# Performance work log

Hardware: AMD Instinct MI355X
Metric: run time of the kernel (lower is better)

The kernel has to match this reference:

```python
import jax, jax.numpy as jnp
import numpy as np

# SMPL-X kinematic tree (55 joints): 22 body, jaw, 2 eyes, 15 left-hand, 15 right-hand
PARENTS = np.array([-1, 0, 0, 0, 1, 2, 3, 4, 5, 6, 7, 8, 9, 9, 9, 12, 13, 14, 16, 17, 18, 19,
                    15, 15, 15,
                    20, 25, 26, 20, 28, 29, 20, 31, 32, 20, 34, 35, 20, 37, 38,
                    21, 40, 41, 21, 43, 44, 21, 46, 47, 21, 49, 50, 21, 52, 53])
V = 10475   # SMPL-X vertex count
J = 55      # joints
NB = 10     # betas
PF = 54 * 9 # pose-feature dim
B, L = 4, 128


def axis_angle_to_matrix(aa):
    # aa: (..., 3) -> (..., 3, 3) via Rodrigues' formula
    angle = jnp.sqrt(jnp.sum(aa * aa, axis=-1, keepdims=True) + 1e-12)  # (...,1)
    axis = aa / angle
    x, y, z = axis[..., 0], axis[..., 1], axis[..., 2]
    zero = jnp.zeros_like(x)
    K = jnp.stack([jnp.stack([zero, -z, y], -1),
                   jnp.stack([z, zero, -x], -1),
                   jnp.stack([-y, x, zero], -1)], axis=-2)           # (...,3,3)
    s = jnp.sin(angle)[..., None]
    c = jnp.cos(angle)[..., None]
    eye = jnp.eye(3, dtype=aa.dtype)
    outer = axis[..., :, None] * axis[..., None, :]
    return c * eye + s * K + (1.0 - c) * outer


def batch_rigid_transform(rot_mats, joints):
    # rot_mats: (..., J, 3, 3), joints: (..., J, 3) -> rel_transforms (..., J, 4, 4)
    rel = jnp.concatenate([joints[..., :1, :],
                           joints[..., 1:, :] - joints[..., PARENTS[1:], :]], axis=-2)
    top = jnp.concatenate([rot_mats, rel[..., None]], axis=-1)        # (...,J,3,4)
    bottom = jnp.broadcast_to(jnp.array([0., 0., 0., 1.], top.dtype),
                              top.shape[:-2] + (1, 4))
    tmats = jnp.concatenate([top, bottom], axis=-2)                   # (...,J,4,4)
    chain = [tmats[..., 0, :, :]]
    for i in range(1, J):  # fixed 55-joint tree dependency
        chain.append(chain[PARENTS[i]] @ tmats[..., i, :, :])
    T = jnp.stack(chain, axis=-3)                                     # (...,J,4,4)
    corr = jnp.einsum('...jcd,...jd->...jc', T[..., :3, :3], joints)
    return T.at[..., :3, 3].add(-corr)


def setup_inputs() -> dict:
    key = jax.random.key(0)
    ks = jax.random.split(key, 11)
    w = jax.random.uniform(ks[8], (V, J), dtype=jnp.float32)
    lbs_weights = w / jnp.sum(w, axis=-1, keepdims=True)
    return {
        'body_pose': 0.3 * jax.random.normal(ks[0], (B, L, 63), jnp.float32),
        'betas': jax.random.normal(ks[1], (B, L, NB), jnp.float32),
        'global_orient': 0.3 * jax.random.normal(ks[2], (B, L, 3), jnp.float32),
        'transl': jax.random.normal(ks[3], (B, L, 3), jnp.float32),
        'v_template': 0.5 * jax.random.normal(ks[4], (V, 3), jnp.float32),
        'shapedirs': 0.01 * jax.random.normal(ks[5], (V, 3, NB), jnp.float32),
        'posedirs': 0.01 * jax.random.normal(ks[6], (PF, V, 3), jnp.float32),
        'lbs_weights': lbs_weights,
        'J_template': 0.3 * jax.random.normal(ks[7], (J, 3), jnp.float32),
        'J_shapedirs': 0.01 * jax.random.normal(ks[9], (J, 3, NB), jnp.float32),
        'other_default_pose': 0.1 * jax.random.normal(ks[10], (99,), jnp.float32),
    }


def reference(body_pose, betas, global_orient, transl, v_template, shapedirs,
              posedirs, lbs_weights, J_template, J_shapedirs, other_default_pose):
    prefix = body_pose.shape[:-1]
    odp = jnp.broadcast_to(other_default_pose, prefix + (99,))
    full_pose = jnp.concatenate([global_orient, body_pose, odp], axis=-1)  # (B,L,165)
    rot_mats = axis_angle_to_matrix(full_pose.reshape(prefix + (J, 3)))    # (B,L,55,3,3)
    # fast skeleton
    joints = J_template + jnp.einsum('...k,jck->...jc', betas, J_shapedirs)  # (B,L,55,3)
    A = batch_rigid_transform(rot_mats, joints)                              # (B,L,55,4,4)
    eye = jnp.eye(3, dtype=rot_mats.dtype)
    pose_feature = (rot_mats[..., 1:, :, :] - eye).reshape(prefix + (PF,))
    v_posed = (v_template
               + jnp.einsum('...k,vck->...vc', betas, shapedirs)
               + jnp.einsum('...k,kvc->...vc', pose_feature, posedirs))      # (B,L,V,3)
    T = jnp.einsum('vj,...jcd->...vcd', lbs_weights, A)                      # (B,L,V,4,4)
    verts = (jnp.einsum('...vcd,...vd->...vc', T[..., :3, :3], v_posed)
             + T[..., :3, 3])
    return verts + transl[..., None, :]
```

## Files before the change

kernel.cpp:

```cpp
#include <hip/hip_runtime.h>

#define V_CNT   10475
#define N3      31425
#define NPAD    31488
#define J_CNT   55
#define NBETA   10
#define KP      512
#define NFRAMES 512
#define BM      64
#define BNC     192
#define VTILES  164
#define FTILES  8

typedef __attribute__((ext_vector_type(8))) __bf16 bf16x8;
typedef __attribute__((ext_vector_type(8))) unsigned short ushort8;
typedef __attribute__((ext_vector_type(4))) float f32x4;

__device__ __forceinline__ unsigned short f2bf(float f) {
    unsigned u = __float_as_uint(f);
    u += 0x7fff + ((u >> 16) & 1);
    return (unsigned short)(u >> 16);
}
__device__ __forceinline__ float bf2f(unsigned short s) {
    return __uint_as_float(((unsigned)s) << 16);
}
__device__ __forceinline__ void gl_lds16(const void* g, void* l) {
    auto gp = (const __attribute__((address_space(1))) unsigned int*)(uintptr_t)g;
    auto lp = (__attribute__((address_space(3))) unsigned int*)(unsigned int)(uintptr_t)l;
    __builtin_amdgcn_global_load_lds(gp, lp, 16, 0, 0);
}

__device__ __constant__ int c_parents[J_CNT] = {
    -1, 0, 0, 0, 1, 2, 3, 4, 5, 6, 7, 8, 9, 9, 9, 12, 13, 14, 16, 17, 18, 19,
    15, 15, 15,
    20, 25, 26, 20, 28, 29, 20, 31, 32, 20, 34, 35, 20, 37, 38,
    21, 40, 41, 21, 43, 44, 21, 46, 47, 21, 49, 50, 21, 52, 53};

__global__ __launch_bounds__(64) void skel_kernel(
    const float* __restrict__ body_pose, const float* __restrict__ betas,
    const float* __restrict__ global_orient, const float* __restrict__ J_template,
    const float* __restrict__ J_shapedirs, const float* __restrict__ odp,
    unsigned short* __restrict__ pf_ext, unsigned short* __restrict__ A_bf)
{
    const int n = blockIdx.x;
    const int lane = threadIdx.x;
    __shared__ float R_s[J_CNT][9];
    __shared__ float j_s[J_CNT][3];
    __shared__ float G_s[J_CNT][12];

    if (lane < J_CNT) {
        float aa0, aa1, aa2;
        if (lane == 0) {
            aa0 = global_orient[n * 3 + 0];
            aa1 = global_orient[n * 3 + 1];
            aa2 = global_orient[n * 3 + 2];
        } else if (lane < 22) {
            int o = n * 63 + (lane - 1) * 3;
            aa0 = body_pose[o]; aa1 = body_pose[o + 1]; aa2 = body_pose[o + 2];
        } else {
            int o = (lane - 22) * 3;
            aa0 = odp[o]; aa1 = odp[o + 1]; aa2 = odp[o + 2];
        }
        float ang = sqrtf(aa0 * aa0 + aa1 * aa1 + aa2 * aa2 + 1e-12f);
        float inv = 1.0f / ang;
        float ax = aa0 * inv, ay = aa1 * inv, az = aa2 * inv;
        float s = sinf(ang), c = cosf(ang), cc = 1.0f - c;
        float R[9];
        R[0] = c + cc * ax * ax;        R[1] = -s * az + cc * ax * ay;  R[2] = s * ay + cc * ax * az;
        R[3] = s * az + cc * ax * ay;   R[4] = c + cc * ay * ay;        R[5] = -s * ax + cc * ay * az;
        R[6] = -s * ay + cc * ax * az;  R[7] = s * ax + cc * ay * az;   R[8] = c + cc * az * az;
#pragma unroll
        for (int k = 0; k < 9; k++) R_s[lane][k] = R[k];
#pragma unroll
        for (int cd = 0; cd < 3; cd++) {
            float acc = J_template[lane * 3 + cd];
#pragma unroll
            for (int k = 0; k < NBETA; k++)
                acc += betas[n * NBETA + k] * J_shapedirs[(lane * 3 + cd) * NBETA + k];
            j_s[lane][cd] = acc;
        }
        if (lane >= 1) {
#pragma unroll
            for (int e = 0; e < 9; e++)
                pf_ext[n * KP + (lane - 1) * 9 + e] =
                    f2bf(R[e] - ((e == 0 || e == 4 || e == 8) ? 1.0f : 0.0f));
        }
    }
    if (lane == 55) {
#pragma unroll
        for (int b = 0; b < NBETA; b++) pf_ext[n * KP + 486 + b] = f2bf(betas[n * NBETA + b]);
        pf_ext[n * KP + 496] = 0x3F80;
    }
    if (lane == 56) {
        for (int k = 497; k < KP; k++) pf_ext[n * KP + k] = 0;
    }
    __syncthreads();
    if (lane == 0) {
        for (int r = 0; r < 3; r++) {
            G_s[0][r * 4 + 0] = R_s[0][r * 3 + 0];
            G_s[0][r * 4 + 1] = R_s[0][r * 3 + 1];
            G_s[0][r * 4 + 2] = R_s[0][r * 3 + 2];
            G_s[0][r * 4 + 3] = j_s[0][r];
        }
        for (int i = 1; i < J_CNT; i++) {
            int p = c_parents[i];
            float rel0 = j_s[i][0] - j_s[p][0];
            float rel1 = j_s[i][1] - j_s[p][1];
            float rel2 = j_s[i][2] - j_s[p][2];
            for (int r = 0; r < 3; r++) {
                float g0 = G_s[p][r * 4 + 0], g1 = G_s[p][r * 4 + 1], g2 = G_s[p][r * 4 + 2];
                G_s[i][r * 4 + 0] = g0 * R_s[i][0] + g1 * R_s[i][3] + g2 * R_s[i][6];
                G_s[i][r * 4 + 1] = g0 * R_s[i][1] + g1 * R_s[i][4] + g2 * R_s[i][7];
                G_s[i][r * 4 + 2] = g0 * R_s[i][2] + g1 * R_s[i][5] + g2 * R_s[i][8];
                G_s[i][r * 4 + 3] = g0 * rel0 + g1 * rel1 + g2 * rel2 + G_s[p][r * 4 + 3];
            }
        }
    }
    __syncthreads();
    float vals[12];
#pragma unroll
    for (int r = 0; r < 12; r++) vals[r] = 0.0f;
    if (lane < J_CNT) {
        const float jx = j_s[lane][0], jy = j_s[lane][1], jz = j_s[lane][2];
#pragma unroll
        for (int r = 0; r < 3; r++) {
            float g0 = G_s[lane][r * 4 + 0], g1 = G_s[lane][r * 4 + 1], g2 = G_s[lane][r * 4 + 2];
            vals[r * 4 + 0] = g0;
            vals[r * 4 + 1] = g1;
            vals[r * 4 + 2] = g2;
            vals[r * 4 + 3] = G_s[lane][r * 4 + 3] - (g0 * jx + g1 * jy + g2 * jz);
        }
    }
#pragma unroll
    for (int r = 0; r < 12; r++)
        A_bf[(n * 12 + r) * 64 + lane] = f2bf(vals[r]);
}

__global__ __launch_bounds__(256) void repack_kernel(
    const float* __restrict__ posedirs, const float* __restrict__ shapedirs,
    const float* __restrict__ v_template, unsigned short* __restrict__ B_pack)
{
    __shared__ float t[64][65];
    const int n0 = blockIdx.x * 64, k0 = blockIdx.y * 64;
    const int tn = threadIdx.x & 63, tk4 = threadIdx.x >> 6;
#pragma unroll
    for (int rep = 0; rep < 16; rep++) {
        int kl = rep * 4 + tk4;
        int kg = k0 + kl, ng = n0 + tn;
        float v = 0.0f;
        if (ng < N3) {
            if (kg < 486)       v = posedirs[(size_t)kg * N3 + ng];
            else if (kg < 496)  v = shapedirs[ng * NBETA + (kg - 486)];
            else if (kg == 496) v = v_template[ng];
        }
        t[kl][tn] = v;
    }
    __syncthreads();
#pragma unroll
    for (int rep = 0; rep < 2; rep++) {
        int nl = rep * 32 + (threadIdx.x >> 3);
        int kg = threadIdx.x & 7;
        ushort8 val;
#pragma unroll
        for (int j = 0; j < 8; j++) val[j] = f2bf(t[kg * 8 + j][nl]);
        *(ushort8*)(&B_pack[(size_t)(n0 + nl) * KP + k0 + kg * 8]) = val;
    }
}

__global__ __launch_bounds__(256, 2) void gemm_kernel(
    const unsigned short* __restrict__ pf_ext, const unsigned short* __restrict__ B_pack,
    const unsigned short* __restrict__ A_bf, const float* __restrict__ lbs_weights,
    const float* __restrict__ transl, float* __restrict__ out)
{
    __shared__ __align__(128) unsigned char smem[74496];
    unsigned char* pf_b0 = smem;
    unsigned char* pf_b1 = smem + 8192;
    unsigned char* B_b0  = smem + 16384;
    unsigned char* B_b1  = smem + 40960;
    unsigned char* w_b   = smem + 65536;
    float* tr_s          = (float*)(smem + 73728);
    unsigned short* vp_s = (unsigned short*)(smem + 16384);
    float* rst           = (float*)(smem + 41472);

    const int tid = threadIdx.x;
    const int w = tid >> 6, l = tid & 63;
    const int wm = w >> 1, wn = w & 1;

    const int bid = blockIdx.x;
    const int group = bid >> 6, gi = bid & 63;
    int vt, ft;
    if (group < 20) { vt = group * 8 + (gi & 7); ft = gi >> 3; }
    else            { vt = 160 + (gi & 3);       ft = gi >> 2; }
    const int f0 = ft * BM;
    const int v00 = vt * 64;
    const int n0c = vt * BNC;

    {
        int v = tid >> 2, jg = tid & 3;
        int vg = v00 + v;
#pragma unroll
        for (int h = 0; h < 2; h++) {
            ushort8 val;
#pragma unroll
            for (int e = 0; e < 8; e++) {
                int j = jg * 16 + h * 8 + e;
                float f = (vg < V_CNT && j < J_CNT) ? lbs_weights[vg * J_CNT + j] : 0.0f;
                val[e] = f2bf(f);
            }
            int chunk = (jg * 2 + h) ^ (v & 7);
            *(ushort8*)(w_b + v * 128 + chunk * 16) = val;
        }
    }
    if (tid < 192) tr_s[tid] = transl[f0 * 3 + tid];

    const unsigned char* pfg = (const unsigned char*)pf_ext + (size_t)f0 * (KP * 2);
    const unsigned char* Bg  = (const unsigned char*)B_pack + (size_t)n0c * (KP * 2);

#define STAGE_KS(ks, pfd, Bd)                                                              \
    {                                                                                      \
        const int kb = (ks) * 128;                                                         \
        _Pragma("unroll")                                                                  \
        for (int i = 0; i < 2; i++) {                                                      \
            int row0 = w * 16 + i * 8;                                                     \
            int row = row0 + (l >> 3);                                                     \
            const unsigned char* src = pfg + (size_t)row * (KP * 2) + kb +                 \
                                       (((l & 7) ^ (l >> 3)) * 16);                        \
            gl_lds16(src, (pfd) + row0 * 128);                                             \
        }                                                                                  \
        _Pragma("unroll")                                                                  \
        for (int i = 0; i < 6; i++) {                                                      \
            int row0 = i * 32 + w * 8;                                                     \
            int row = row0 + (l >> 3);                                                     \
            const unsigned char* src = Bg + (size_t)row * (KP * 2) + kb +                  \
                                       (((l & 7) ^ (l >> 3)) * 16);                        \
            gl_lds16(src, (Bd) + row0 * 128);                                              \
        }                                                                                  \
    }

    f32x4 acc[2][6];
#pragma unroll
    for (int m = 0; m < 2; m++)
#pragma unroll
        for (int nn = 0; nn < 6; nn++) acc[m][nn] = (f32x4){0.f, 0.f, 0.f, 0.f};

    STAGE_KS(0, pf_b0, B_b0);
    STAGE_KS(1, pf_b1, B_b1);
    asm volatile("s_waitcnt vmcnt(8)" ::: "memory");
    __builtin_amdgcn_sched_barrier(0);
    __builtin_amdgcn_s_barrier();

#pragma unroll
    for (int ks = 0; ks < 8; ks++) {
        unsigned char* pfc = (ks & 1) ? pf_b1 : pf_b0;
        unsigned char* Bc  = (ks & 1) ? B_b1 : B_b0;
#pragma unroll
        for (int ksub = 0; ksub < 2; ksub++) {
            bf16x8 a[2], b[6];
#pragma unroll
            for (int m = 0; m < 2; m++) {
                int f = wm * 32 + m * 16 + (l & 15);
                int off = f * 128 + ((ksub * 64 + (l >> 4) * 16) ^ ((f & 7) << 4));
                a[m] = *(const bf16x8*)(pfc + off);
            }
#pragma unroll
            for (int nn = 0; nn < 6; nn++) {
                int col = wn * 96 + nn * 16 + (l & 15);
                int off = col * 128 + ((ksub * 64 + (l >> 4) * 16) ^ ((col & 7) << 4));
                b[nn] = *(const bf16x8*)(Bc + off);
            }
#pragma unroll
            for (int m = 0; m < 2; m++)
#pragma unroll
                for (int nn = 0; nn < 6; nn++)
                    acc[m][nn] = __builtin_amdgcn_mfma_f32_16x16x32_bf16(a[m], b[nn], acc[m][nn], 0, 0, 0);
        }
        __builtin_amdgcn_sched_barrier(0);
        __builtin_amdgcn_s_barrier();
        if (ks < 6) {
            STAGE_KS(ks + 2, pfc, Bc);
        }
        if (ks < 7) {
            if (ks < 6) asm volatile("s_waitcnt vmcnt(8)" ::: "memory");
            else        asm volatile("s_waitcnt vmcnt(0)" ::: "memory");
            __builtin_amdgcn_sched_barrier(0);
            __builtin_amdgcn_s_barrier();
        }
    }
#undef STAGE_KS

#pragma unroll
    for (int m = 0; m < 2; m++)
#pragma unroll
        for (int nn = 0; nn < 6; nn++)
#pragma unroll
            for (int e = 0; e < 4; e++) {
                int f = wm * 32 + m * 16 + (l >> 4) * 4 + e;
                int col = wn * 96 + nn * 16 + (l & 15);
                vp_s[f * 196 + col] = f2bf(acc[m][nn][e]);
            }
    __syncthreads();

    const unsigned char* Ab = (const unsigned char*)A_bf;
    float res[3][8][2];
#pragma unroll
    for (int c = 0; c < 3; c++) {
        f32x4 acc2[8][2];
#pragma unroll
        for (int m = 0; m < 8; m++)
#pragma unroll
            for (int nn = 0; nn < 2; nn++) acc2[m][nn] = (f32x4){0.f, 0.f, 0.f, 0.f};
#pragma unroll
        for (int ksub = 0; ksub < 2; ksub++) {
            bf16x8 bw[2];
#pragma unroll
            for (int nn = 0; nn < 2; nn++) {
                int v = wn * 32 + nn * 16 + (l & 15);
                int off = v * 128 + ((ksub * 64 + (l >> 4) * 16) ^ ((v & 7) << 4));
                bw[nn] = *(const bf16x8*)(w_b + off);
            }
#pragma unroll
            for (int m = 0; m < 8; m++) {
                int row16 = l & 15;
                int f_rel = m * 4 + (row16 >> 2);
                int rr = row16 & 3;
                const unsigned char* asrc = Ab +
                    ((size_t)((f0 + wm * 32 + f_rel) * 12 + c * 4 + rr)) * 128 +
                    ksub * 64 + (l >> 4) * 16;
                bf16x8 af = *(const bf16x8*)asrc;
                acc2[m][0] = __builtin_amdgcn_mfma_f32_16x16x32_bf16(af, bw[0], acc2[m][0], 0, 0, 0);
                acc2[m][1] = __builtin_amdgcn_mfma_f32_16x16x32_bf16(af, bw[1], acc2[m][1], 0, 0, 0);
            }
        }
#pragma unroll
        for (int m = 0; m < 8; m++)
#pragma unroll
            for (int nn = 0; nn < 2; nn++) {
                int f_rel = wm * 32 + m * 4 + (l >> 4);
                int vloc = wn * 32 + nn * 16 + (l & 15);
                float d0 = bf2f(vp_s[f_rel * 196 + vloc * 3 + 0]);
                float d1 = bf2f(vp_s[f_rel * 196 + vloc * 3 + 1]);
                float d2 = bf2f(vp_s[f_rel * 196 + vloc * 3 + 2]);
                f32x4 tt = acc2[m][nn];
                res[c][m][nn] = tt[0] * d0 + tt[1] * d1 + tt[2] * d2 + tt[3] + tr_s[f_rel * 3 + c];
            }
    }

    const int olim = N3 - v00 * 3;
#pragma unroll
    for (int chunk = 0; chunk < 2; chunk++) {
        __syncthreads();
        if (wm == chunk) {
#pragma unroll
            for (int m = 0; m < 8; m++)
#pragma unroll
                for (int nn = 0; nn < 2; nn++) {
                    int r = m * 4 + (l >> 4);
                    int colv = (wn * 32 + nn * 16 + (l & 15)) * 3;
#pragma unroll
                    for (int c = 0; c < 3; c++)
                        rst[r * 200 + colv + c] = res[c][m][nn];
                }
        }
        __syncthreads();
        size_t base = ((size_t)(f0 + chunk * 32) * V_CNT + v00) * 3;
#pragma unroll
        for (int k = 0; k < 24; k++) {
            int i = tid + k * 256;
            int r = i / 192;
            int o = i - r * 192;
            if (o < olim)
                out[base + (size_t)r * N3 + o] = rst[r * 200 + o];
        }
    }
}

extern "C" void kernel_launch(void* const* d_in, const int* in_sizes, int n_in,
                              void* d_out, int out_size, void* d_ws, size_t ws_size,
                              hipStream_t stream)
{
    const float* body_pose     = (const float*)d_in[0];
    const float* betas         = (const float*)d_in[1];
    const float* global_orient = (const float*)d_in[2];
    const float* transl        = (const float*)d_in[3];
    const float* v_template    = (const float*)d_in[4];
    const float* shapedirs     = (const float*)d_in[5];
    const float* posedirs      = (const float*)d_in[6];
    const float* lbs_weights   = (const float*)d_in[7];
    const float* J_template    = (const float*)d_in[8];
    const float* J_shapedirs   = (const float*)d_in[9];
    const float* odp           = (const float*)d_in[10];
    float* out = (float*)d_out;

    unsigned short* B_pack = (unsigned short*)d_ws;
    unsigned short* pf_ext = (unsigned short*)((char*)d_ws + 32243712);
    unsigned short* A_bf   = (unsigned short*)((char*)d_ws + 32243712 + 524288);

    dim3 rgrid(NPAD / 64, KP / 64);
    repack_kernel<<<rgrid, 256, 0, stream>>>(posedirs, shapedirs, v_template, B_pack);

    skel_kernel<<<NFRAMES, 64, 0, stream>>>(body_pose, betas, global_orient,
                                            J_template, J_shapedirs, odp,
                                            pf_ext, A_bf);

    gemm_kernel<<<VTILES * FTILES, 256, 0, stream>>>(pf_ext, B_pack, A_bf, lbs_weights,
                                                     transl, out);
}
```

Measured before the change: 116.5 us.

## Load pose-feature operand directly into registers and shrink shared memory footprint

```diff
diff --git a/kernel.cpp b/kernel.cpp
--- a/kernel.cpp
+++ b/kernel.cpp
@@ -172,15 +172,13 @@
     const unsigned short* __restrict__ A_bf, const float* __restrict__ lbs_weights,
     const float* __restrict__ transl, float* __restrict__ out)
 {
-    __shared__ __align__(128) unsigned char smem[74496];
-    unsigned char* pf_b0 = smem;
-    unsigned char* pf_b1 = smem + 8192;
-    unsigned char* B_b0  = smem + 16384;
-    unsigned char* B_b1  = smem + 40960;
-    unsigned char* w_b   = smem + 65536;
-    float* tr_s          = (float*)(smem + 73728);
-    unsigned short* vp_s = (unsigned short*)(smem + 16384);
-    float* rst           = (float*)(smem + 41472);
+    __shared__ __align__(128) unsigned char smem[49920];
+    unsigned char* B_b0  = smem;
+    unsigned char* B_b1  = smem + 24576;
+    float* tr_s          = (float*)(smem + 49152);
+    unsigned short* vp_s = (unsigned short*)(smem);
+    unsigned char* w_b   = smem + 25600;
+    float* rst           = (float*)(smem);
 
     const int tid = threadIdx.x;
     const int w = tid >> 6, l = tid & 63;
@@ -195,38 +193,14 @@
     const int v00 = vt * 64;
     const int n0c = vt * BNC;
 
-    {
-        int v = tid >> 2, jg = tid & 3;
-        int vg = v00 + v;
-#pragma unroll
-        for (int h = 0; h < 2; h++) {
-            ushort8 val;
-#pragma unroll
-            for (int e = 0; e < 8; e++) {
-                int j = jg * 16 + h * 8 + e;
-                float f = (vg < V_CNT && j < J_CNT) ? lbs_weights[vg * J_CNT + j] : 0.0f;
-                val[e] = f2bf(f);
-            }
-            int chunk = (jg * 2 + h) ^ (v & 7);
-            *(ushort8*)(w_b + v * 128 + chunk * 16) = val;
-        }
-    }
     if (tid < 192) tr_s[tid] = transl[f0 * 3 + tid];
 
     const unsigned char* pfg = (const unsigned char*)pf_ext + (size_t)f0 * (KP * 2);
     const unsigned char* Bg  = (const unsigned char*)B_pack + (size_t)n0c * (KP * 2);
 
-#define STAGE_KS(ks, pfd, Bd)                                                              \
+#define STAGE_B(ks, Bd)                                                                    \
     {                                                                                      \
         const int kb = (ks) * 128;                                                         \
-        _Pragma("unroll")                                                                  \
-        for (int i = 0; i < 2; i++) {                                                      \
-            int row0 = w * 16 + i * 8;                                                     \
-            int row = row0 + (l >> 3);                                                     \
-            const unsigned char* src = pfg + (size_t)row * (KP * 2) + kb +                 \
-                                       (((l & 7) ^ (l >> 3)) * 16);                        \
-            gl_lds16(src, (pfd) + row0 * 128);                                             \
-        }                                                                                  \
         _Pragma("unroll")                                                                  \
         for (int i = 0; i < 6; i++) {                                                      \
             int row0 = i * 32 + w * 8;                                                     \
@@ -236,6 +210,17 @@
             gl_lds16(src, (Bd) + row0 * 128);                                              \
         }                                                                                  \
     }
+#define PF_LOAD(ks, dst)                                                                   \
+    {                                                                                      \
+        _Pragma("unroll")                                                                  \
+        for (int m = 0; m < 2; m++)                                                        \
+            _Pragma("unroll")                                                              \
+            for (int ksub = 0; ksub < 2; ksub++) {                                         \
+                int row = wm * 32 + m * 16 + (l & 15);                                     \
+                (dst)[m][ksub] = *(const bf16x8*)(pfg + (size_t)row * 1024 +               \
+                                                  (ks) * 128 + ksub * 64 + (l >> 4) * 16); \
+            }                                                                              \
+    }
 
     f32x4 acc[2][6];
 #pragma unroll
@@ -243,25 +228,22 @@
 #pragma unroll
         for (int nn = 0; nn < 6; nn++) acc[m][nn] = (f32x4){0.f, 0.f, 0.f, 0.f};
 
-    STAGE_KS(0, pf_b0, B_b0);
-    STAGE_KS(1, pf_b1, B_b1);
-    asm volatile("s_waitcnt vmcnt(8)" ::: "memory");
+    bf16x8 pfR[2][2][2];
+
+    PF_LOAD(0, pfR[0]);
+    PF_LOAD(1, pfR[1]);
+    STAGE_B(0, B_b0);
+    STAGE_B(1, B_b1);
+    asm volatile("s_waitcnt vmcnt(6)" ::: "memory");
     __builtin_amdgcn_sched_barrier(0);
     __builtin_amdgcn_s_barrier();
 
 #pragma unroll
     for (int ks = 0; ks < 8; ks++) {
-        unsigned char* pfc = (ks & 1) ? pf_b1 : pf_b0;
-        unsigned char* Bc  = (ks & 1) ? B_b1 : B_b0;
+        unsigned char* Bc = (ks & 1) ? B_b1 : B_b0;
 #pragma unroll
         for (int ksub = 0; ksub < 2; ksub++) {
-            bf16x8 a[2], b[6];
-#pragma unroll
-            for (int m = 0; m < 2; m++) {
-                int f = wm * 32 + m * 16 + (l & 15);
-                int off = f * 128 + ((ksub * 64 + (l >> 4) * 16) ^ ((f & 7) << 4));
-                a[m] = *(const bf16x8*)(pfc + off);
-            }
+            bf16x8 b[6];
 #pragma unroll
             for (int nn = 0; nn < 6; nn++) {
                 int col = wn * 96 + nn * 16 + (l & 15);
@@ -272,22 +254,41 @@
             for (int m = 0; m < 2; m++)
 #pragma unroll
                 for (int nn = 0; nn < 6; nn++)
-                    acc[m][nn] = __builtin_amdgcn_mfma_f32_16x16x32_bf16(a[m], b[nn], acc[m][nn], 0, 0, 0);
+                    acc[m][nn] = __builtin_amdgcn_mfma_f32_16x16x32_bf16(
+                        pfR[ks & 1][m][ksub], b[nn], acc[m][nn], 0, 0, 0);
         }
         __builtin_amdgcn_sched_barrier(0);
         __builtin_amdgcn_s_barrier();
         if (ks < 6) {
-            STAGE_KS(ks + 2, pfc, Bc);
+            PF_LOAD(ks + 2, pfR[ks & 1]);
+            STAGE_B(ks + 2, Bc);
         }
         if (ks < 7) {
-            if (ks < 6) asm volatile("s_waitcnt vmcnt(8)" ::: "memory");
+            if (ks < 6) asm volatile("s_waitcnt vmcnt(6)" ::: "memory");
             else        asm volatile("s_waitcnt vmcnt(0)" ::: "memory");
             __builtin_amdgcn_sched_barrier(0);
             __builtin_amdgcn_s_barrier();
         }
     }
-#undef STAGE_KS
-
+#undef STAGE_B
+#undef PF_LOAD
+
+    {
+        int v = tid >> 2, jg = tid & 3;
+        int vg = v00 + v;
+#pragma unroll
+        for (int h = 0; h < 2; h++) {
+            ushort8 val;
+#pragma unroll
+            for (int e = 0; e < 8; e++) {
+                int j = jg * 16 + h * 8 + e;
+                float f = (vg < V_CNT && j < J_CNT) ? lbs_weights[vg * J_CNT + j] : 0.0f;
+                val[e] = f2bf(f);
+            }
+            int chunk = (jg * 2 + h) ^ (v & 7);
+            *(ushort8*)(w_b + v * 128 + chunk * 16) = val;
+        }
+    }
 #pragma unroll
     for (int m = 0; m < 2; m++)
 #pragma unroll
```

Result: slower. 143.0 us (+22.7%).

## Merge repack and skeleton kernels into one launch and defer weight staging

Applied to the files above, without the earlier changes.

```diff
diff --git a/kernel.cpp b/kernel.cpp
--- a/kernel.cpp
+++ b/kernel.cpp
@@ -11,6 +11,7 @@
 #define BNC     192
 #define VTILES  164
 #define FTILES  8
+#define RPK_BLOCKS (492 * 8)
 
 typedef __attribute__((ext_vector_type(8))) __bf16 bf16x8;
 typedef __attribute__((ext_vector_type(8))) unsigned short ushort8;
@@ -36,17 +37,48 @@
     20, 25, 26, 20, 28, 29, 20, 31, 32, 20, 34, 35, 20, 37, 38,
     21, 40, 41, 21, 43, 44, 21, 46, 47, 21, 49, 50, 21, 52, 53};
 
-__global__ __launch_bounds__(64) void skel_kernel(
+__global__ __launch_bounds__(256) void prep_kernel(
+    const float* __restrict__ posedirs, const float* __restrict__ shapedirs,
+    const float* __restrict__ v_template, unsigned short* __restrict__ B_pack,
     const float* __restrict__ body_pose, const float* __restrict__ betas,
     const float* __restrict__ global_orient, const float* __restrict__ J_template,
     const float* __restrict__ J_shapedirs, const float* __restrict__ odp,
     unsigned short* __restrict__ pf_ext, unsigned short* __restrict__ A_bf)
 {
-    const int n = blockIdx.x;
-    const int lane = threadIdx.x;
+    const int rb = blockIdx.x;
+    const int tid = threadIdx.x;
+
     __shared__ float R_s[J_CNT][9];
     __shared__ float j_s[J_CNT][3];
     __shared__ float G_s[J_CNT][12];
+
+    if (rb < RPK_BLOCKS) {
+        const int n0 = (rb % 492) * 64;
+        const int k0 = (rb / 492) * 64;
+        const int nl = tid >> 2;
+        const int kh = tid & 3;
+        const int ng = n0 + nl;
+        ushort8 v0, v1;
+#pragma unroll
+        for (int j = 0; j < 16; j++) {
+            int kgl = k0 + kh * 16 + j;
+            float v = 0.0f;
+            if (ng < N3) {
+                if (kgl < 486)       v = posedirs[(size_t)kgl * N3 + ng];
+                else if (kgl < 496)  v = shapedirs[ng * NBETA + (kgl - 486)];
+                else if (kgl == 496) v = v_template[ng];
+            }
+            if (j < 8) v0[j] = f2bf(v);
+            else       v1[j - 8] = f2bf(v);
+        }
+        unsigned short* dst = &B_pack[(size_t)(n0 + nl) * KP + k0 + kh * 16];
+        *(ushort8*)(dst)     = v0;
+        *(ushort8*)(dst + 8) = v1;
+        return;
+    }
+
+    const int n = rb - RPK_BLOCKS;
+    const int lane = tid;
 
     if (lane < J_CNT) {
         float aa0, aa1, aa2;
@@ -117,53 +149,24 @@
         }
     }
     __syncthreads();
-    float vals[12];
-#pragma unroll
-    for (int r = 0; r < 12; r++) vals[r] = 0.0f;
-    if (lane < J_CNT) {
-        const float jx = j_s[lane][0], jy = j_s[lane][1], jz = j_s[lane][2];
-#pragma unroll
-        for (int r = 0; r < 3; r++) {
-            float g0 = G_s[lane][r * 4 + 0], g1 = G_s[lane][r * 4 + 1], g2 = G_s[lane][r * 4 + 2];
-            vals[r * 4 + 0] = g0;
-            vals[r * 4 + 1] = g1;
-            vals[r * 4 + 2] = g2;
-            vals[r * 4 + 3] = G_s[lane][r * 4 + 3] - (g0 * jx + g1 * jy + g2 * jz);
-        }
-    }
-#pragma unroll
-    for (int r = 0; r < 12; r++)
-        A_bf[(n * 12 + r) * 64 + lane] = f2bf(vals[r]);
-}
-
-__global__ __launch_bounds__(256) void repack_kernel(
-    const float* __restrict__ posedirs, const float* __restrict__ shapedirs,
-    const float* __restrict__ v_template, unsigned short* __restrict__ B_pack)
-{
-    __shared__ float t[64][65];
-    const int n0 = blockIdx.x * 64, k0 = blockIdx.y * 64;
-    const int tn = threadIdx.x & 63, tk4 = threadIdx.x >> 6;
-#pragma unroll
-    for (int rep = 0; rep < 16; rep++) {
-        int kl = rep * 4 + tk4;
-        int kg = k0 + kl, ng = n0 + tn;
-        float v = 0.0f;
-        if (ng < N3) {
-            if (kg < 486)       v = posedirs[(size_t)kg * N3 + ng];
-            else if (kg < 496)  v = shapedirs[ng * NBETA + (kg - 486)];
-            else if (kg == 496) v = v_template[ng];
-        }
-        t[kl][tn] = v;
-    }
-    __syncthreads();
-#pragma unroll
-    for (int rep = 0; rep < 2; rep++) {
-        int nl = rep * 32 + (threadIdx.x >> 3);
-        int kg = threadIdx.x & 7;
-        ushort8 val;
-#pragma unroll
-        for (int j = 0; j < 8; j++) val[j] = f2bf(t[kg * 8 + j][nl]);
-        *(ushort8*)(&B_pack[(size_t)(n0 + nl) * KP + k0 + kg * 8]) = val;
+    if (lane < 64) {
+        float vals[12];
+#pragma unroll
+        for (int r = 0; r < 12; r++) vals[r] = 0.0f;
+        if (lane < J_CNT) {
+            const float jx = j_s[lane][0], jy = j_s[lane][1], jz = j_s[lane][2];
+#pragma unroll
+            for (int r = 0; r < 3; r++) {
+                float g0 = G_s[lane][r * 4 + 0], g1 = G_s[lane][r * 4 + 1], g2 = G_s[lane][r * 4 + 2];
+                vals[r * 4 + 0] = g0;
+                vals[r * 4 + 1] = g1;
+                vals[r * 4 + 2] = g2;
+                vals[r * 4 + 3] = G_s[lane][r * 4 + 3] - (g0 * jx + g1 * jy + g2 * jz);
+            }
+        }
+#pragma unroll
+        for (int r = 0; r < 12; r++)
+            A_bf[(n * 12 + r) * 64 + lane] = f2bf(vals[r]);
     }
 }
 
@@ -194,24 +197,6 @@
     const int f0 = ft * BM;
     const int v00 = vt * 64;
     const int n0c = vt * BNC;
-
-    {
-        int v = tid >> 2, jg = tid & 3;
-        int vg = v00 + v;
-#pragma unroll
-        for (int h = 0; h < 2; h++) {
-            ushort8 val;
-#pragma unroll
-            for (int e = 0; e < 8; e++) {
-                int j = jg * 16 + h * 8 + e;
-                float f = (vg < V_CNT && j < J_CNT) ? lbs_weights[vg * J_CNT + j] : 0.0f;
-                val[e] = f2bf(f);
-            }
-            int chunk = (jg * 2 + h) ^ (v & 7);
-            *(ushort8*)(w_b + v * 128 + chunk * 16) = val;
-        }
-    }
-    if (tid < 192) tr_s[tid] = transl[f0 * 3 + tid];
 
     const unsigned char* pfg = (const unsigned char*)pf_ext + (size_t)f0 * (KP * 2);
     const unsigned char* Bg  = (const unsigned char*)B_pack + (size_t)n0c * (KP * 2);
@@ -288,6 +273,24 @@
     }
 #undef STAGE_KS
 
+    {
+        int v = tid >> 2, jg = tid & 3;
+        int vg = v00 + v;
+#pragma unroll
+        for (int h = 0; h < 2; h++) {
+            ushort8 val;
+#pragma unroll
+            for (int e = 0; e < 8; e++) {
+                int j = jg * 16 + h * 8 + e;
+                float f = (vg < V_CNT && j < J_CNT) ? lbs_weights[vg * J_CNT + j] : 0.0f;
+                val[e] = f2bf(f);
+            }
+            int chunk = (jg * 2 + h) ^ (v & 7);
+            *(ushort8*)(w_b + v * 128 + chunk * 16) = val;
+        }
+    }
+    if (tid < 192) tr_s[tid] = transl[f0 * 3 + tid];
+
 #pragma unroll
     for (int m = 0; m < 2; m++)
 #pragma unroll
@@ -395,12 +398,10 @@
     unsigned short* pf_ext = (unsigned short*)((char*)d_ws + 32243712);
     unsigned short* A_bf   = (unsigned short*)((char*)d_ws + 32243712 + 524288);
 
-    dim3 rgrid(NPAD / 64, KP / 64);
-    repack_kernel<<<rgrid, 256, 0, stream>>>(posedirs, shapedirs, v_template, B_pack);
-
-    skel_kernel<<<NFRAMES, 64, 0, stream>>>(body_pose, betas, global_orient,
-                                            J_template, J_shapedirs, odp,
-                                            pf_ext, A_bf);
+    prep_kernel<<<RPK_BLOCKS + NFRAMES, 256, 0, stream>>>(
+        posedirs, shapedirs, v_template, B_pack,
+        body_pose, betas, global_orient, J_template, J_shapedirs, odp,
+        pf_ext, A_bf);
 
     gemm_kernel<<<VTILES * FTILES, 256, 0, stream>>>(pf_ext, B_pack, A_bf, lbs_weights,
                                                      transl, out);
```

Result: no change. 117.3 us (+0.7%).

## Double frame tile per block to reuse B tile across two frame halves

Applied to the files above, without the earlier changes.

```diff
diff --git a/kernel.cpp b/kernel.cpp
--- a/kernel.cpp
+++ b/kernel.cpp
@@ -7,10 +7,10 @@
 #define NBETA   10
 #define KP      512
 #define NFRAMES 512
-#define BM      64
+#define BMF     128
 #define BNC     192
 #define VTILES  164
-#define FTILES  8
+#define FPAIRS  4
 
 typedef __attribute__((ext_vector_type(8))) __bf16 bf16x8;
 typedef __attribute__((ext_vector_type(8))) unsigned short ushort8;
@@ -172,46 +172,28 @@
     const unsigned short* __restrict__ A_bf, const float* __restrict__ lbs_weights,
     const float* __restrict__ transl, float* __restrict__ out)
 {
-    __shared__ __align__(128) unsigned char smem[74496];
+    __shared__ __align__(128) unsigned char smem[81920];
     unsigned char* pf_b0 = smem;
-    unsigned char* pf_b1 = smem + 8192;
-    unsigned char* B_b0  = smem + 16384;
-    unsigned char* B_b1  = smem + 40960;
-    unsigned char* w_b   = smem + 65536;
-    float* tr_s          = (float*)(smem + 73728);
-    unsigned short* vp_s = (unsigned short*)(smem + 16384);
-    float* rst           = (float*)(smem + 41472);
+    unsigned char* pf_b1 = smem + 16384;
+    unsigned char* B_b0  = smem + 32768;
+    unsigned char* B_b1  = smem + 57344;
+    unsigned char* w_b   = smem;
+    float* tr_s          = (float*)(smem + 8192);
+    unsigned short* vp_s = (unsigned short*)(smem + 30720);
+    float* rst           = (float*)(smem + 55808);
 
     const int tid = threadIdx.x;
     const int w = tid >> 6, l = tid & 63;
     const int wm = w >> 1, wn = w & 1;
 
     const int bid = blockIdx.x;
-    const int group = bid >> 6, gi = bid & 63;
-    int vt, ft;
-    if (group < 20) { vt = group * 8 + (gi & 7); ft = gi >> 3; }
-    else            { vt = 160 + (gi & 3);       ft = gi >> 2; }
-    const int f0 = ft * BM;
+    const int group = bid >> 5, gi = bid & 31;
+    int vt, fp;
+    if (group < 20) { vt = group * 8 + (gi & 7); fp = gi >> 3; }
+    else            { vt = 160 + (gi & 3);       fp = gi >> 2; }
+    const int f0 = fp * BMF;
     const int v00 = vt * 64;
     const int n0c = vt * BNC;
-
-    {
-        int v = tid >> 2, jg = tid & 3;
-        int vg = v00 + v;
-#pragma unroll
-        for (int h = 0; h < 2; h++) {
-            ushort8 val;
-#pragma unroll
-            for (int e = 0; e < 8; e++) {
-                int j = jg * 16 + h * 8 + e;
-                float f = (vg < V_CNT && j < J_CNT) ? lbs_weights[vg * J_CNT + j] : 0.0f;
-                val[e] = f2bf(f);
-            }
-            int chunk = (jg * 2 + h) ^ (v & 7);
-            *(ushort8*)(w_b + v * 128 + chunk * 16) = val;
-        }
-    }
-    if (tid < 192) tr_s[tid] = transl[f0 * 3 + tid];
 
     const unsigned char* pfg = (const unsigned char*)pf_ext + (size_t)f0 * (KP * 2);
     const unsigned char* Bg  = (const unsigned char*)B_pack + (size_t)n0c * (KP * 2);
@@ -220,8 +202,8 @@
     {                                                                                      \
         const int kb = (ks) * 128;                                                         \
         _Pragma("unroll")                                                                  \
-        for (int i = 0; i < 2; i++) {                                                      \
-            int row0 = w * 16 + i * 8;                                                     \
+        for (int i = 0; i < 4; i++) {                                                      \
+            int row0 = w * 32 + i * 8;                                                     \
             int row = row0 + (l >> 3);                                                     \
             const unsigned char* src = pfg + (size_t)row * (KP * 2) + kb +                 \
                                        (((l & 7) ^ (l >> 3)) * 16);                        \
@@ -237,15 +219,17 @@
         }                                                                                  \
     }
 
-    f32x4 acc[2][6];
-#pragma unroll
-    for (int m = 0; m < 2; m++)
-#pragma unroll
-        for (int nn = 0; nn < 6; nn++) acc[m][nn] = (f32x4){0.f, 0.f, 0.f, 0.f};
+    f32x4 acc[2][2][6];
+#pragma unroll
+    for (int h = 0; h < 2; h++)
+#pragma unroll
+        for (int m = 0; m < 2; m++)
+#pragma unroll
+            for (int nn = 0; nn < 6; nn++) acc[h][m][nn] = (f32x4){0.f, 0.f, 0.f, 0.f};
 
     STAGE_KS(0, pf_b0, B_b0);
     STAGE_KS(1, pf_b1, B_b1);
-    asm volatile("s_waitcnt vmcnt(8)" ::: "memory");
+    asm volatile("s_waitcnt vmcnt(10)" ::: "memory");
     __builtin_amdgcn_sched_barrier(0);
     __builtin_amdgcn_s_barrier();
 
@@ -255,13 +239,15 @@
         unsigned char* Bc  = (ks & 1) ? B_b1 : B_b0;
 #pragma unroll
         for (int ksub = 0; ksub < 2; ksub++) {
-            bf16x8 a[2], b[6];
-#pragma unroll
-            for (int m = 0; m < 2; m++) {
-                int f = wm * 32 + m * 16 + (l & 15);
-                int off = f * 128 + ((ksub * 64 + (l >> 4) * 16) ^ ((f & 7) << 4));
-                a[m] = *(const bf16x8*)(pfc + off);
-            }
+            bf16x8 a[2][2], b[6];
+#pragma unroll
+            for (int h = 0; h < 2; h++)
+#pragma unroll
+                for (int m = 0; m < 2; m++) {
+                    int f = h * 64 + wm * 32 + m * 16 + (l & 15);
+                    int off = f * 128 + ((ksub * 64 + (l >> 4) * 16) ^ ((f & 7) << 4));
+                    a[h][m] = *(const bf16x8*)(pfc + off);
+                }
 #pragma unroll
             for (int nn = 0; nn < 6; nn++) {
                 int col = wn * 96 + nn * 16 + (l & 15);
@@ -269,10 +255,13 @@
                 b[nn] = *(const bf16x8*)(Bc + off);
             }
 #pragma unroll
-            for (int m = 0; m < 2; m++)
-#pragma unroll
-                for (int nn = 0; nn < 6; nn++)
-                    acc[m][nn] = __builtin_amdgcn_mfma_f32_16x16x32_bf16(a[m], b[nn], acc[m][nn], 0, 0, 0);
+            for (int h = 0; h < 2; h++)
+#pragma unroll
+                for (int m = 0; m < 2; m++)
+#pragma unroll
+                    for (int nn = 0; nn < 6; nn++)
+                        acc[h][m][nn] = __builtin_amdgcn_mfma_f32_16x16x32_bf16(
+                            a[h][m], b[nn], acc[h][m][nn], 0, 0, 0);
         }
         __builtin_amdgcn_sched_barrier(0);
         __builtin_amdgcn_s_barrier();
@@ -280,7 +269,7 @@
             STAGE_KS(ks + 2, pfc, Bc);
         }
         if (ks < 7) {
-            if (ks < 6) asm volatile("s_waitcnt vmcnt(8)" ::: "memory");
+            if (ks < 6) asm volatile("s_waitcnt vmcnt(10)" ::: "memory");
             else        asm volatile("s_waitcnt vmcnt(0)" ::: "memory");
             __builtin_amdgcn_sched_barrier(0);
             __builtin_amdgcn_s_barrier();
@@ -288,89 +277,115 @@
     }
 #undef STAGE_KS
 
-#pragma unroll
-    for (int m = 0; m < 2; m++)
-#pragma unroll
-        for (int nn = 0; nn < 6; nn++)
-#pragma unroll
-            for (int e = 0; e < 4; e++) {
-                int f = wm * 32 + m * 16 + (l >> 4) * 4 + e;
-                int col = wn * 96 + nn * 16 + (l & 15);
-                vp_s[f * 196 + col] = f2bf(acc[m][nn][e]);
-            }
-    __syncthreads();
+    {
+        int v = tid >> 2, jg = tid & 3;
+        int vg = v00 + v;
+#pragma unroll
+        for (int h = 0; h < 2; h++) {
+            ushort8 val;
+#pragma unroll
+            for (int e = 0; e < 8; e++) {
+                int j = jg * 16 + h * 8 + e;
+                float f = (vg < V_CNT && j < J_CNT) ? lbs_weights[vg * J_CNT + j] : 0.0f;
+                val[e] = f2bf(f);
+            }
+            int chunk = (jg * 2 + h) ^ (v & 7);
+            *(ushort8*)(w_b + v * 128 + chunk * 16) = val;
+        }
+    }
+#pragma unroll
+    for (int i = tid; i < 384; i += 256) tr_s[i] = transl[f0 * 3 + i];
 
     const unsigned char* Ab = (const unsigned char*)A_bf;
-    float res[3][8][2];
-#pragma unroll
-    for (int c = 0; c < 3; c++) {
-        f32x4 acc2[8][2];
-#pragma unroll
-        for (int m = 0; m < 8; m++)
-#pragma unroll
-            for (int nn = 0; nn < 2; nn++) acc2[m][nn] = (f32x4){0.f, 0.f, 0.f, 0.f};
-#pragma unroll
-        for (int ksub = 0; ksub < 2; ksub++) {
-            bf16x8 bw[2];
-#pragma unroll
-            for (int nn = 0; nn < 2; nn++) {
-                int v = wn * 32 + nn * 16 + (l & 15);
-                int off = v * 128 + ((ksub * 64 + (l >> 4) * 16) ^ ((v & 7) << 4));
-                bw[nn] = *(const bf16x8*)(w_b + off);
-            }
-#pragma unroll
-            for (int m = 0; m < 8; m++) {
-                int row16 = l & 15;
-                int f_rel = m * 4 + (row16 >> 2);
-                int rr = row16 & 3;
-                const unsigned char* asrc = Ab +
-                    ((size_t)((f0 + wm * 32 + f_rel) * 12 + c * 4 + rr)) * 128 +
-                    ksub * 64 + (l >> 4) * 16;
-                bf16x8 af = *(const bf16x8*)asrc;
-                acc2[m][0] = __builtin_amdgcn_mfma_f32_16x16x32_bf16(af, bw[0], acc2[m][0], 0, 0, 0);
-                acc2[m][1] = __builtin_amdgcn_mfma_f32_16x16x32_bf16(af, bw[1], acc2[m][1], 0, 0, 0);
-            }
-        }
-#pragma unroll
-        for (int m = 0; m < 8; m++)
-#pragma unroll
-            for (int nn = 0; nn < 2; nn++) {
-                int f_rel = wm * 32 + m * 4 + (l >> 4);
-                int vloc = wn * 32 + nn * 16 + (l & 15);
-                float d0 = bf2f(vp_s[f_rel * 196 + vloc * 3 + 0]);
-                float d1 = bf2f(vp_s[f_rel * 196 + vloc * 3 + 1]);
-                float d2 = bf2f(vp_s[f_rel * 196 + vloc * 3 + 2]);
-                f32x4 tt = acc2[m][nn];
-                res[c][m][nn] = tt[0] * d0 + tt[1] * d1 + tt[2] * d2 + tt[3] + tr_s[f_rel * 3 + c];
-            }
-    }
-
     const int olim = N3 - v00 * 3;
-#pragma unroll
-    for (int chunk = 0; chunk < 2; chunk++) {
+
+#pragma unroll 1
+    for (int h = 0; h < 2; h++) {
+#pragma unroll
+        for (int m = 0; m < 2; m++)
+#pragma unroll
+            for (int nn = 0; nn < 6; nn++)
+#pragma unroll
+                for (int e = 0; e < 4; e++) {
+                    int f = wm * 32 + m * 16 + (l >> 4) * 4 + e;
+                    int col = wn * 96 + nn * 16 + (l & 15);
+                    vp_s[f * 196 + col] = f2bf(acc[h][m][nn][e]);
+                }
         __syncthreads();
-        if (wm == chunk) {
+
+        const int f0h = f0 + h * 64;
+        float res[3][8][2];
+#pragma unroll
+        for (int c = 0; c < 3; c++) {
+            f32x4 acc2[8][2];
 #pragma unroll
             for (int m = 0; m < 8; m++)
 #pragma unroll
+                for (int nn = 0; nn < 2; nn++) acc2[m][nn] = (f32x4){0.f, 0.f, 0.f, 0.f};
+#pragma unroll
+            for (int ksub = 0; ksub < 2; ksub++) {
+                bf16x8 bw[2];
+#pragma unroll
                 for (int nn = 0; nn < 2; nn++) {
-                    int r = m * 4 + (l >> 4);
-                    int colv = (wn * 32 + nn * 16 + (l & 15)) * 3;
-#pragma unroll
-                    for (int c = 0; c < 3; c++)
-                        rst[r * 200 + colv + c] = res[c][m][nn];
+                    int v = wn * 32 + nn * 16 + (l & 15);
+                    int off = v * 128 + ((ksub * 64 + (l >> 4) * 16) ^ ((v & 7) << 4));
+                    bw[nn] = *(const bf16x8*)(w_b + off);
                 }
+#pragma unroll
+                for (int m = 0; m < 8; m++) {
+                    int row16 = l & 15;
+                    int f_rel = m * 4 + (row16 >> 2);
+                    int rr = row16 & 3;
+                    const unsigned char* asrc = Ab +
+                        ((size_t)((f0h + wm * 32 + f_rel) * 12 + c * 4 + rr)) * 128 +
+                        ksub * 64 + (l >> 4) * 16;
+                    bf16x8 af = *(const bf16x8*)asrc;
+                    acc2[m][0] = __builtin_amdgcn_mfma_f32_16x16x32_bf16(af, bw[0], acc2[m][0], 0, 0, 0);
+                    acc2[m][1] = __builtin_amdgcn_mfma_f32_16x16x32_bf16(af, bw[1], acc2[m][1], 0, 0, 0);
+                }
+            }
+#pragma unroll
+            for (int m = 0; m < 8; m++)
+#pragma unroll
+                for (int nn = 0; nn < 2; nn++) {
+                    int f_rel = wm * 32 + m * 4 + (l >> 4);
+                    int vloc = wn * 32 + nn * 16 + (l & 15);
+                    float d0 = bf2f(vp_s[f_rel * 196 + vloc * 3 + 0]);
+                    float d1 = bf2f(vp_s[f_rel * 196 + vloc * 3 + 1]);
+                    float d2 = bf2f(vp_s[f_rel * 196 + vloc * 3 + 2]);
+                    f32x4 tt = acc2[m][nn];
+                    res[c][m][nn] = tt[0] * d0 + tt[1] * d1 + tt[2] * d2 + tt[3]
+                                    + tr_s[(h * 64 + f_rel) * 3 + c];
+                }
+        }
+
+#pragma unroll
+        for (int chunk = 0; chunk < 2; chunk++) {
+            __syncthreads();
+            if (wm == chunk) {
+#pragma unroll
+                for (int m = 0; m < 8; m++)
+#pragma unroll
+                    for (int nn = 0; nn < 2; nn++) {
+                        int r = m * 4 + (l >> 4);
+                        int colv = (wn * 32 + nn * 16 + (l & 15)) * 3;
+#pragma unroll
+                        for (int c = 0; c < 3; c++)
+                            rst[r * 200 + colv + c] = res[c][m][nn];
+                    }
+            }
+            __syncthreads();
+            size_t base = ((size_t)(f0h + chunk * 32) * V_CNT + v00) * 3;
+#pragma unroll
+            for (int k = 0; k < 24; k++) {
+                int i = tid + k * 256;
+                int r = i / 192;
+                int o = i - r * 192;
+                if (o < olim)
+                    out[base + (size_t)r * N3 + o] = rst[r * 200 + o];
+            }
         }
         __syncthreads();
-        size_t base = ((size_t)(f0 + chunk * 32) * V_CNT + v00) * 3;
-#pragma unroll
-        for (int k = 0; k < 24; k++) {
-            int i = tid + k * 256;
-            int r = i / 192;
-            int o = i - r * 192;
-            if (o < olim)
-                out[base + (size_t)r * N3 + o] = rst[r * 200 + o];
-        }
     }
 }
 
@@ -402,6 +417,6 @@
                                             J_template, J_shapedirs, odp,
                                             pf_ext, A_bf);
 
-    gemm_kernel<<<VTILES * FTILES, 256, 0, stream>>>(pf_ext, B_pack, A_bf, lbs_weights,
-                                                     transl, out);
-}
+    gemm_kernel<<<20 * 32 + 16, 256, 0, stream>>>(pf_ext, B_pack, A_bf, lbs_weights,
+                                                  transl, out);
+}
```

New measurement: 272.6 us. +133.9%, slower.
